# Kernel tuning notes

Measured on AMD Instinct MI355X. Metric: run time of the kernel, lower is better.

The kernel has to match this reference:

```python
import jax, jax.numpy as jnp
import numpy as np
from jax import lax

H_HEADS = 8      # attention heads
C_HID = 32       # per-head channels
NEG_SLOPE = 0.2  # PyG GATConv default leaky_relu slope


def _gat(x, src, dst, W, a_src, a_dst, b, num_nodes):
    # x: (N, Din); src/dst: (E',) with self-loops already appended
    h = (x @ W).reshape(num_nodes, H_HEADS, C_HID)          # (N, H, C)
    e = jax.nn.leaky_relu((h * a_src).sum(-1)[src] + (h * a_dst).sum(-1)[dst], NEG_SLOPE)  # (E', H)
    emax = jax.ops.segment_max(e, dst, num_segments=num_nodes)
    ex = jnp.exp(e - emax[dst])
    denom = jax.ops.segment_sum(ex, dst, num_segments=num_nodes)
    alpha = ex / (denom[dst] + 1e-16)                        # segment softmax over incoming edges
    out = jax.ops.segment_sum(h[src] * alpha[:, :, None], dst, num_segments=num_nodes)
    return out.reshape(num_nodes, H_HEADS * C_HID) + b


def _lstm_dir(seq, Wih, Whh, bih, bhh):
    # seq: (K, D); single-direction LSTM, returns final hidden state (Hs,)
    Hs = Whh.shape[1]
    def step(carry, x):
        h, c = carry
        g = x @ Wih.T + h @ Whh.T + bih + bhh                # (4*Hs,)
        i, f, gg, o = jnp.split(g, 4)
        c = jax.nn.sigmoid(f) * c + jax.nn.sigmoid(i) * jnp.tanh(gg)
        h = jax.nn.sigmoid(o) * jnp.tanh(c)
        return (h, c), None
    (h, _), _ = lax.scan(step, (jnp.zeros(Hs, seq.dtype), jnp.zeros(Hs, seq.dtype)), seq)
    return h


def setup_inputs():
    key = jax.random.key(0)
    ks = jax.random.split(key, 20)
    K, N, E = 8, 10000, 160000
    D1, D2, LH = 1, H_HEADS * C_HID, 256   # D2 = 256
    s = 0.1
    inp = {}
    inp['xs'] = jax.random.normal(ks[0], (K, N, D1), jnp.float32)
    inp['edge_index'] = jax.random.randint(ks[1], (K, 2, E), 0, N, jnp.int32)
    inp['W1'] = jax.random.normal(ks[2], (D1, D2), jnp.float32) * s
    inp['a_src1'] = jax.random.normal(ks[3], (H_HEADS, C_HID), jnp.float32) * s
    inp['a_dst1'] = jax.random.normal(ks[4], (H_HEADS, C_HID), jnp.float32) * s
    inp['b1'] = jnp.zeros((D2,), jnp.float32)
    inp['W2'] = jax.random.normal(ks[5], (D2, D2), jnp.float32) * s
    inp['a_src2'] = jax.random.normal(ks[6], (H_HEADS, C_HID), jnp.float32) * s
    inp['a_dst2'] = jax.random.normal(ks[7], (H_HEADS, C_HID), jnp.float32) * s
    inp['b2'] = jnp.zeros((D2,), jnp.float32)
    inp['Wih_f'] = jax.random.normal(ks[8], (4 * LH, D2), jnp.float32) * s
    inp['Whh_f'] = jax.random.normal(ks[9], (4 * LH, LH), jnp.float32) * s
    inp['bih_f'] = jnp.zeros((4 * LH,), jnp.float32)
    inp['bhh_f'] = jnp.zeros((4 * LH,), jnp.float32)
    inp['Wih_b'] = jax.random.normal(ks[10], (4 * LH, D2), jnp.float32) * s
    inp['Whh_b'] = jax.random.normal(ks[11], (4 * LH, LH), jnp.float32) * s
    inp['bih_b'] = jnp.zeros((4 * LH,), jnp.float32)
    inp['bhh_b'] = jnp.zeros((4 * LH,), jnp.float32)
    return inp


def reference(xs, edge_index, W1, a_src1, a_dst1, b1, W2, a_src2, a_dst2, b2,
              Wih_f, Whh_f, bih_f, bhh_f, Wih_b, Whh_b, bih_b, bhh_b):
    N = xs.shape[1]
    loops = jnp.arange(N, dtype=edge_index.dtype)  # self-loops (PyG default)
    def snap(carry, inp):
        x, ei = inp
        src = jnp.concatenate([ei[0], loops])
        dst = jnp.concatenate([ei[1], loops])
        h = jax.nn.relu(_gat(x, src, dst, W1, a_src1, a_dst1, b1, N))
        h = jax.nn.relu(_gat(h, src, dst, W2, a_src2, a_dst2, b2, N))
        return carry, h.mean(0)   # global mean pool -> (256,)
    _, embs = lax.scan(snap, 0, (xs, edge_index))   # (K, 256)
    h_fwd = _lstm_dir(embs, Wih_f, Whh_f, bih_f, bhh_f)
    h_bwd = _lstm_dir(embs[::-1], Wih_b, Whh_b, bih_b, bhh_b)
    return jnp.concatenate([h_fwd, h_bwd])[None, :]  # (1, 512)
```

## Files before the change

### kernel.cpp

```cpp
#include <hip/hip_runtime.h>
#include <math.h>

#define H_HEADS 8
#define C_HID 32
#define D2 256
#define NEG_SLOPE 0.2f
#define KSTEPS 8

__device__ __forceinline__ float lrelu(float x) { return x < 0.f ? NEG_SLOPE * x : x; }
__device__ __forceinline__ float sigmoidf(float x) { return 1.f / (1.f + expf(-x)); }


__global__ void zero_all_kernel(int* counts, int* fill, double* embp, int KN, int NEMBP,
                                const float* __restrict__ W1, const float* __restrict__ a_src1,
                                const float* __restrict__ a_dst1, float* Pvec, int D1) {
    int tid = blockIdx.x * blockDim.x + threadIdx.x;
    if (tid < KN) { counts[tid] = 0; fill[tid] = 0; }
    if (tid < NEMBP) embp[tid] = 0.0;
    if (blockIdx.x == 0 && threadIdx.x < 16 && D1 == 1) {
        int h = threadIdx.x & 7;
        const float* a = (threadIdx.x >= 8) ? a_dst1 : a_src1;
        float s = 0.f;
        for (int c = 0; c < 32; ++c) s += W1[h * 32 + c] * a[h * 32 + c];
        Pvec[threadIdx.x] = s;
    }
}


__global__ void count_all_kernel(const int* __restrict__ ei, int E, int N, int K,
                                 int* __restrict__ counts) {
    int bid = blockIdx.x;
    int k = bid % K;
    int jb = bid / K;
    int j = jb * blockDim.x + threadIdx.x;
    if (j >= E + N) return;
    int d = (j < E) ? ei[(size_t)k * 2 * E + E + j] : (j - E);
    atomicAdd(&counts[(size_t)k * N + d], 1);
}

__global__ __launch_bounds__(1024) void scan_all_kernel(const int* __restrict__ counts,
                                                        int* __restrict__ row_ptr, int N) {
    int k = blockIdx.x;
    const int* cnt = counts + (size_t)k * N;
    int* rp = row_ptr + (size_t)k * (N + 1);
    __shared__ int part[1024];
    int t = threadIdx.x;
    int ipt = (N + 1023) >> 10;
    int begin = t * ipt;
    int end = begin + ipt; if (end > N) end = N;
    if (begin > N) begin = N;
    int s = 0;
    for (int i = begin; i < end; ++i) s += cnt[i];
    part[t] = s;
    __syncthreads();
    for (int d = 1; d < 1024; d <<= 1) {
        int v = 0;
        if (t >= d) v = part[t - d];
        __syncthreads();
        if (t >= d) part[t] += v;
        __syncthreads();
    }
    int run = (t == 0) ? 0 : part[t - 1];
    for (int i = begin; i < end; ++i) { rp[i] = run; run += cnt[i]; }
    if (t == 1023) rp[N] = part[1023];
}

__global__ void scatter_all_kernel(const int* __restrict__ ei, int E, int N, int K,
                                   const int* __restrict__ row_ptr, int* __restrict__ fill,
                                   int* __restrict__ ein) {
    int bid = blockIdx.x;
    int k = bid % K;
    int jb = bid / K;
    int j = jb * blockDim.x + threadIdx.x;
    if (j >= E + N) return;
    int s, d;
    if (j < E) { s = ei[(size_t)k * 2 * E + j]; d = ei[(size_t)k * 2 * E + E + j]; }
    else { s = j - E; d = s; }
    int pos = row_ptr[(size_t)k * (N + 1) + d] + atomicAdd(&fill[(size_t)k * N + d], 1);
    ein[(size_t)k * (E + N) + pos] = s;
}


__global__ __launch_bounds__(256) void agg1_all_kernel(const float* __restrict__ xs,
                                                       const float* __restrict__ P,
                                                       const int* __restrict__ row_ptr,
                                                       const int* __restrict__ ein,
                                                       const float* __restrict__ W1,
                                                       const float* __restrict__ b1,
                                                       float* __restrict__ bufB,
                                                       int N, int E2, int k0, int BKcur) {
    int bid = blockIdx.x;
    int kb = bid % BKcur;
    int nb = bid / BKcur;
    int k = k0 + kb;
    const float* x = xs + (size_t)k * N;
    const int* rp = row_ptr + (size_t)k * (N + 1);
    const int* ek = ein + (size_t)k * E2;
    float* out = bufB + (size_t)kb * N * 256;

    int n = nb * 4 + (threadIdx.x >> 6);
    if (n >= N) return;
    int lane = threadIdx.x & 63;
    int e0 = rp[n], e1 = rp[n + 1];
    int h8 = lane & 7;
    float Ps = P[h8], Pd = P[8 + h8];
    float base = x[n] * Pd;

    float mx = -INFINITY;
    for (int i = e0 + (lane >> 3); i < e1; i += 8) {
        float xv = x[ek[i]];
        mx = fmaxf(mx, lrelu(xv * Ps + base));
    }
    mx = fmaxf(mx, __shfl_xor(mx, 8));
    mx = fmaxf(mx, __shfl_xor(mx, 16));
    mx = fmaxf(mx, __shfl_xor(mx, 32));

    float num = 0.f, den = 0.f;
    for (int i = e0 + (lane >> 3); i < e1; i += 8) {
        float xv = x[ek[i]];
        float w = expf(lrelu(xv * Ps + base) - mx);
        num += w * xv;
        den += w;
    }
    num += __shfl_xor(num, 8);  den += __shfl_xor(den, 8);
    num += __shfl_xor(num, 16); den += __shfl_xor(den, 16);
    num += __shfl_xor(num, 32); den += __shfl_xor(den, 32);
    float S = num / (den + 1e-16f);

    int hd = lane >> 3;
    float Sh = __shfl(S, hd);
    const float4 wv = *(const float4*)(W1 + lane * 4);
    const float4 bv = *(const float4*)(b1 + lane * 4);
    float4 o;
    o.x = fmaxf(Sh * wv.x + bv.x, 0.f);
    o.y = fmaxf(Sh * wv.y + bv.y, 0.f);
    o.z = fmaxf(Sh * wv.z + bv.z, 0.f);
    o.w = fmaxf(Sh * wv.w + bv.w, 0.f);
    *(float4*)(out + (size_t)n * 256 + lane * 4) = o;
}


__global__ void h1_kernel(const float* __restrict__ x, const float* __restrict__ W,
                          float* __restrict__ h, int N, int D1) {
    int tid = blockIdx.x * blockDim.x + threadIdx.x;
    if (tid >= N * 256) return;
    int n = tid >> 8, j = tid & 255;
    float acc = 0.f;
    for (int d = 0; d < D1; ++d) acc += x[n * D1 + d] * W[d * 256 + j];
    h[tid] = acc;
}

__global__ __launch_bounds__(256) void s_all_kernel(const float* __restrict__ bufA,
                                                    const float* __restrict__ a_src,
                                                    const float* __restrict__ a_dst,
                                                    float* __restrict__ s_src,
                                                    float* __restrict__ s_dst, int N) {
    int kb = blockIdx.y;
    int j = blockIdx.x * 256 + threadIdx.x;
    if (j >= N * 8) return;
    int n = j >> 3, hh = j & 7;
    const float* hp = bufA + (size_t)kb * N * 256 + (size_t)n * 256 + hh * 32;
    const float* as = a_src + hh * 32;
    const float* ad = a_dst + hh * 32;
    float ss = 0.f, sd = 0.f;
#pragma unroll
    for (int c = 0; c < 32; ++c) { float v = hp[c]; ss += v * as[c]; sd += v * ad[c]; }
    s_src[(size_t)kb * N * 8 + j] = ss;
    s_dst[(size_t)kb * N * 8 + j] = sd;
}

__global__ __launch_bounds__(256) void agg2_out_kernel(const float* __restrict__ h,
                                                       const float* __restrict__ s_src,
                                                       const float* __restrict__ s_dst,
                                                       const int* __restrict__ row_ptr,
                                                       const int* __restrict__ ein,
                                                       const float* __restrict__ bias,
                                                       float* __restrict__ out,
                                                       int N, int E2, int k0) {
    int k = k0;
    const int* rp = row_ptr + (size_t)k * (N + 1);
    const int* ek = ein + (size_t)k * E2;
    int n = blockIdx.x * 4 + (threadIdx.x >> 6);
    if (n >= N) return;
    int lane = threadIdx.x & 63;
    int e0 = rp[n], e1 = rp[n + 1];
    int h8 = lane & 7;
    float sd8 = s_dst[n * 8 + h8];

    float mx = -INFINITY;
    for (int i = e0 + (lane >> 3); i < e1; i += 8) {
        int s = ek[i];
        mx = fmaxf(mx, lrelu(s_src[s * 8 + h8] + sd8));
    }
    mx = fmaxf(mx, __shfl_xor(mx, 8));
    mx = fmaxf(mx, __shfl_xor(mx, 16));
    mx = fmaxf(mx, __shfl_xor(mx, 32));

    int hd = lane >> 3;
    float m = __shfl(mx, hd);
    float sdh = __shfl(sd8, hd);

    float den = 0.f;
    float4 acc = make_float4(0.f, 0.f, 0.f, 0.f);
    for (int i = e0; i < e1; ++i) {
        int s = ek[i];
        const float4 hv = *(const float4*)(h + (size_t)s * 256 + lane * 4);
        float w = expf(lrelu(s_src[s * 8 + hd] + sdh) - m);
        den += w;
        acc.x += w * hv.x; acc.y += w * hv.y; acc.z += w * hv.z; acc.w += w * hv.w;
    }
    float dE = den + 1e-16f;
    const float4 bv = *(const float4*)(bias + lane * 4);
    float4 o;
    o.x = fmaxf(acc.x / dE + bv.x, 0.f);
    o.y = fmaxf(acc.y / dE + bv.y, 0.f);
    o.z = fmaxf(acc.z / dE + bv.z, 0.f);
    o.w = fmaxf(acc.w / dE + bv.w, 0.f);
    *(float4*)(out + (size_t)n * 256 + lane * 4) = o;
}


__global__ __launch_bounds__(256) void agg2pool_kernel(const float* __restrict__ bufA,
                                                       const float* __restrict__ s_src,
                                                       const float* __restrict__ s_dst,
                                                       const int* __restrict__ row_ptr,
                                                       const int* __restrict__ ein,
                                                       const float* __restrict__ bias,
                                                       double* __restrict__ embp,
                                                       int N, int E2, int k0, int BKcur) {
    int bid = blockIdx.x;
    int kb = bid % BKcur;
    int nb = bid / BKcur;
    int k = k0 + kb;
    int w = threadIdx.x >> 6;
    int lane = threadIdx.x & 63;
    int n = nb * 4 + w;
    bool active = (n < N);
    const float* h = bufA + (size_t)kb * N * 256;
    const float* ssrc = s_src + (size_t)kb * N * 8;
    const float* sdst = s_dst + (size_t)kb * N * 8;
    const int* rp = row_ptr + (size_t)k * (N + 1);
    const int* ek = ein + (size_t)k * E2;

    float4 o = make_float4(0.f, 0.f, 0.f, 0.f);
    if (active) {
        int e0 = rp[n], e1 = rp[n + 1];
        int h8 = lane & 7;
        int es = lane >> 3;
        int hd = lane >> 3;
        float sd8 = sdst[n * 8 + h8];

        float mx = -INFINITY;
        for (int i = e0 + es; i < e1; i += 8) {
            int s = ek[i];
            mx = fmaxf(mx, lrelu(ssrc[s * 8 + h8] + sd8));
        }
        mx = fmaxf(mx, __shfl_xor(mx, 8));
        mx = fmaxf(mx, __shfl_xor(mx, 16));
        mx = fmaxf(mx, __shfl_xor(mx, 32));

        float den = 0.f;
        float4 acc = make_float4(0.f, 0.f, 0.f, 0.f);
        int hd4 = hd;

        for (int c0 = e0; c0 < e1; c0 += 8) {
            int eI = c0 + es;
            bool valid = (eI < e1);
            int sA = ek[valid ? eI : e0];
            float wv = expf(lrelu(ssrc[sA * 8 + h8] + sd8) - mx);
            if (!valid) wv = 0.f;

            int jmax = e1 - c0; if (jmax > 8) jmax = 8;
#pragma unroll 8
            for (int j = 0; j < 8; ++j) {
                if (j >= jmax) break;
                int srcLane = (j << 3) + hd4;
                float wj = __shfl(wv, srcLane);
                int sj = __shfl(sA, srcLane);
                const float4 hv = *(const float4*)(h + (size_t)sj * 256 + lane * 4);
                den += wj;
                acc.x += wj * hv.x;
                acc.y += wj * hv.y;
                acc.z += wj * hv.z;
                acc.w += wj * hv.w;
            }
        }
        float dE = den + 1e-16f;
        const float4 bv = *(const float4*)(bias + lane * 4);
        o.x = fmaxf(acc.x / dE + bv.x, 0.f);
        o.y = fmaxf(acc.y / dE + bv.y, 0.f);
        o.z = fmaxf(acc.z / dE + bv.z, 0.f);
        o.w = fmaxf(acc.w / dE + bv.w, 0.f);
    }

    __shared__ double pe[4][256];
    pe[w][lane * 4 + 0] = (double)o.x;
    pe[w][lane * 4 + 1] = (double)o.y;
    pe[w][lane * 4 + 2] = (double)o.z;
    pe[w][lane * 4 + 3] = (double)o.w;
    __syncthreads();
    int tid = threadIdx.x;
    double s = pe[0][tid] + pe[1][tid] + pe[2][tid] + pe[3][tid];
    atomicAdd(&embp[((size_t)k * 32 + (nb & 31)) * 256 + tid], s);
}


__global__ __launch_bounds__(256) void gemm_kernel(const float* __restrict__ A,
                                                   const float* __restrict__ B,
                                                   float* __restrict__ C, int M) {
    __shared__ float Ast[8][132];
    __shared__ float Bs[8][128];
    int tid = threadIdx.x;
    int bm = blockIdx.x, bn = blockIdx.y;
    int ty = tid >> 4, tx = tid & 15;
    int r0 = ty * 8, c0 = tx * 8;
    float acc[8][8] = {};
    int arow = tid >> 1, acol = (tid & 1) * 4;
    int brow = tid >> 5, bcol = (tid & 31) * 4;
    const float* Bbase = B + bn * 128;

    for (int kt = 0; kt < 256; kt += 8) {
        int gr = bm * 128 + arow;
        float4 av = (gr < M) ? *(const float4*)(A + (size_t)gr * 256 + kt + acol)
                             : make_float4(0.f, 0.f, 0.f, 0.f);
        Ast[acol + 0][arow] = av.x;
        Ast[acol + 1][arow] = av.y;
        Ast[acol + 2][arow] = av.z;
        Ast[acol + 3][arow] = av.w;
        *(float4*)&Bs[brow][bcol] = *(const float4*)(Bbase + (size_t)(kt + brow) * 256 + bcol);
        __syncthreads();
#pragma unroll
        for (int kk = 0; kk < 8; ++kk) {
            float4 a0 = *(const float4*)&Ast[kk][r0];
            float4 a1 = *(const float4*)&Ast[kk][r0 + 4];
            float4 b0 = *(const float4*)&Bs[kk][c0];
            float4 b1 = *(const float4*)&Bs[kk][c0 + 4];
            float ar[8] = {a0.x, a0.y, a0.z, a0.w, a1.x, a1.y, a1.z, a1.w};
            float br[8] = {b0.x, b0.y, b0.z, b0.w, b1.x, b1.y, b1.z, b1.w};
#pragma unroll
            for (int i2 = 0; i2 < 8; ++i2)
#pragma unroll
                for (int j2 = 0; j2 < 8; ++j2) acc[i2][j2] += ar[i2] * br[j2];
        }
        __syncthreads();
    }
#pragma unroll
    for (int i2 = 0; i2 < 8; ++i2) {
        int gm = bm * 128 + r0 + i2;
        if (gm < M) {
            *(float4*)(C + (size_t)gm * 256 + bn * 128 + c0) =
                make_float4(acc[i2][0], acc[i2][1], acc[i2][2], acc[i2][3]);
            *(float4*)(C + (size_t)gm * 256 + bn * 128 + c0 + 4) =
                make_float4(acc[i2][4], acc[i2][5], acc[i2][6], acc[i2][7]);
        }
    }
}


__global__ void merge_kernel(const double* __restrict__ embp, float* __restrict__ emb,
                             int* __restrict__ flags) {
    int k = blockIdx.x, c = threadIdx.x;
    double s = 0.0;
#pragma unroll
    for (int p = 0; p < 32; ++p) s += embp[((size_t)k * 32 + p) * 256 + c];
    emb[k * 256 + c] = (float)s;
    if (blockIdx.x == 0 && threadIdx.x < 2 * (KSTEPS + 1)) flags[threadIdx.x] = 0;
}


__global__ __launch_bounds__(256) void lstm_rec_kernel(
    const float* __restrict__ emb, float invN,
    const float* __restrict__ Wih_f, const float* __restrict__ Whh_f,
    const float* __restrict__ bih_f, const float* __restrict__ bhh_f,
    const float* __restrict__ Wih_b, const float* __restrict__ Whh_b,
    const float* __restrict__ bih_b, const float* __restrict__ bhh_b,
    float* __restrict__ hbuf,
    int* __restrict__ flags,
    float* __restrict__ out) {
    int dir = blockIdx.x >> 4;
    int seg = blockIdx.x & 15;
    const float* Wih = dir ? Wih_b : Wih_f;
    const float* Whh = dir ? Whh_b : Whh_f;
    const float* bih = dir ? bih_b : bih_f;
    const float* bhh = dir ? bhh_b : bhh_f;

    __shared__ float wh[64 * 256];
    __shared__ float wi[64 * 256];
    __shared__ float xs_s[KSTEPS * 256];
    __shared__ float gx[KSTEPS][64];
    __shared__ float garr[64];
    __shared__ float hprev_s[256];
    int tid = threadIdx.x;

    for (int v = tid; v < 64 * 64; v += 256) {
        int lrow = v >> 6;
        int c4 = (v & 63) * 4;
        int grow = ((lrow >> 4) << 8) + seg * 16 + (lrow & 15);
        *(float4*)&wh[lrow * 256 + c4] = *(const float4*)(Whh + (size_t)grow * 256 + c4);
        *(float4*)&wi[lrow * 256 + c4] = *(const float4*)(Wih + (size_t)grow * 256 + c4);
    }
    for (int idx = tid; idx < KSTEPS * 256; idx += 256) xs_s[idx] = emb[idx] * invN;
    __syncthreads();

    for (int d = tid; d < KSTEPS * 64; d += 256) {
        int st = d >> 6, lr = d & 63;
        const float* wr = &wi[lr << 8];
        const float* xr = &xs_s[st << 8];
        int r = (tid & 63) << 2;
        float acc = 0.f;
#pragma unroll 8
        for (int kk = 0; kk < 256; kk += 4) {
            int k2 = (kk + r) & 255;
            acc += wr[k2] * xr[k2] + wr[k2 + 1] * xr[k2 + 1] +
                   wr[k2 + 2] * xr[k2 + 2] + wr[k2 + 3] * xr[k2 + 3];
        }
        int grow = ((lr >> 4) << 8) + seg * 16 + (lr & 15);
        gx[st][lr] = acc + bih[grow] + bhh[grow];
    }

    int* flag = flags + dir * (KSTEPS + 1);
    float* hb = hbuf + dir * (KSTEPS + 1) * 256;

    if (tid < 16)
        __hip_atomic_store(&hb[seg * 16 + tid], 0.f, __ATOMIC_RELAXED, __HIP_MEMORY_SCOPE_AGENT);
    __syncthreads();
    if (tid == 0)
        __hip_atomic_fetch_add(&flag[0], 1, __ATOMIC_RELEASE, __HIP_MEMORY_SCOPE_AGENT);

    float c_reg = 0.f;

    for (int step = 0; step < KSTEPS; ++step) {
        if (tid == 0) {
            while (__hip_atomic_load(&flag[step], __ATOMIC_RELAXED, __HIP_MEMORY_SCOPE_AGENT) < 16) {
                __builtin_amdgcn_s_sleep(1);
            }
            (void)__hip_atomic_load(&flag[step], __ATOMIC_ACQUIRE, __HIP_MEMORY_SCOPE_AGENT);
        }
        __syncthreads();
        hprev_s[tid] = __hip_atomic_load(&hb[step * 256 + tid], __ATOMIC_RELAXED,
                                         __HIP_MEMORY_SCOPE_AGENT);
        __syncthreads();

        int d = tid >> 2, p = tid & 3;
        const float* wr = &wh[(d << 8) + (p << 6)];
        const float* hr = &hprev_s[p << 6];
        int rot = tid & 63;
        float acc = 0.f;
#pragma unroll 8
        for (int k = 0; k < 64; ++k) {
            int k2 = (k + rot) & 63;
            acc += wr[k2] * hr[k2];
        }
        acc += __shfl_xor(acc, 1);
        acc += __shfl_xor(acc, 2);
        if (p == 0) garr[d] = acc;
        __syncthreads();

        if (tid < 16) {
            float ig = sigmoidf(garr[tid] + gx[step][tid]);
            float fg = sigmoidf(garr[16 + tid] + gx[step][16 + tid]);
            float gg = tanhf(garr[32 + tid] + gx[step][32 + tid]);
            float og = sigmoidf(garr[48 + tid] + gx[step][48 + tid]);
            float cn = fg * c_reg + ig * gg;
            c_reg = cn;
            float hn = og * tanhf(cn);
            __hip_atomic_store(&hb[(step + 1) * 256 + seg * 16 + tid], hn, __ATOMIC_RELAXED,
                               __HIP_MEMORY_SCOPE_AGENT);
        }
        __syncthreads();
        if (tid == 0)
            __hip_atomic_fetch_add(&flag[step + 1], 1, __ATOMIC_RELEASE, __HIP_MEMORY_SCOPE_AGENT);
    }

    if (tid < 16)
        out[dir * 256 + seg * 16 + tid] =
            __hip_atomic_load(&hb[KSTEPS * 256 + seg * 16 + tid], __ATOMIC_RELAXED,
                              __HIP_MEMORY_SCOPE_AGENT);
}


extern "C" void kernel_launch(void* const* d_in, const int* in_sizes, int n_in,
                              void* d_out, int out_size, void* d_ws, size_t ws_size,
                              hipStream_t stream) {
    const float* xs = (const float*)d_in[0];
    const int* edge_index = (const int*)d_in[1];
    const float* W1 = (const float*)d_in[2];
    const float* a_src1 = (const float*)d_in[3];
    const float* a_dst1 = (const float*)d_in[4];
    const float* b1 = (const float*)d_in[5];
    const float* W2 = (const float*)d_in[6];
    const float* a_src2 = (const float*)d_in[7];
    const float* a_dst2 = (const float*)d_in[8];
    const float* b2 = (const float*)d_in[9];
    const float* Wih_f = (const float*)d_in[10];
    const float* Whh_f = (const float*)d_in[11];
    const float* bih_f = (const float*)d_in[12];
    const float* bhh_f = (const float*)d_in[13];
    const float* Wih_b = (const float*)d_in[14];
    const float* Whh_b = (const float*)d_in[15];
    const float* bih_b = (const float*)d_in[16];
    const float* bhh_b = (const float*)d_in[17];

    const int K = KSTEPS;
    int D1 = in_sizes[2] / D2;
    int N = in_sizes[0] / (K * D1);
    int E = in_sizes[1] / (2 * K);
    int E2 = E + N;

    auto al = [](size_t x) { return (x + 255) & ~(size_t)255; };
    size_t fixed_sz = al((size_t)K * N * 4)
                    + al((size_t)K * (N + 1) * 4)
                    + al((size_t)K * N * 4)
                    + al((size_t)K * E2 * 4)
                    + al((size_t)K * 32 * 256 * 8)
                    + al((size_t)K * 256 * 4)
                    + al((size_t)2 * (K + 1) * 256 * 4)
                    + al((size_t)2 * (K + 1) * 4)
                    + al(16 * 4);
    int BK = 8;
    while (BK > 1) {
        size_t need = fixed_sz + 2 * al((size_t)BK * N * 8 * 4) + 2 * al((size_t)BK * N * 256 * 4);
        if (need <= ws_size) break;
        BK >>= 1;
    }

    char* w = (char*)d_ws;
    auto alloc = [&](size_t bytes) { char* p = w; w += (bytes + 255) & ~(size_t)255; return p; };
    int* counts = (int*)alloc((size_t)K * N * 4);
    int* row_ptr = (int*)alloc((size_t)K * (N + 1) * 4);
    int* fill = (int*)alloc((size_t)K * N * 4);
    int* ein = (int*)alloc((size_t)K * E2 * 4);
    double* embp = (double*)alloc((size_t)K * 32 * 256 * 8);
    float* emb = (float*)alloc((size_t)K * 256 * 4);
    float* hbuf = (float*)alloc((size_t)2 * (K + 1) * 256 * 4);
    int* flags = (int*)alloc((size_t)2 * (K + 1) * 4);
    float* Pvec = (float*)alloc(16 * 4);
    float* s_src = (float*)alloc((size_t)BK * N * 8 * 4);
    float* s_dst = (float*)alloc((size_t)BK * N * 8 * 4);
    float* bufA = (float*)alloc((size_t)BK * N * 256 * 4);
    float* bufB = (float*)alloc((size_t)BK * N * 256 * 4);

    int KN = K * N;
    int NEMBP = K * 32 * 256;
    int zblk = ((KN > NEMBP ? KN : NEMBP) + 255) / 256;
    zero_all_kernel<<<zblk, 256, 0, stream>>>(counts, fill, embp, KN, NEMBP,
                                              W1, a_src1, a_dst1, Pvec, D1);
    int eblk = (E2 + 255) / 256;
    count_all_kernel<<<eblk * K, 256, 0, stream>>>(edge_index, E, N, K, counts);
    scan_all_kernel<<<K, 1024, 0, stream>>>(counts, row_ptr, N);
    scatter_all_kernel<<<eblk * K, 256, 0, stream>>>(edge_index, E, N, K, row_ptr, fill, ein);

    int nblk4 = (N + 3) / 4;
    int sblk = (N * 8 + 255) / 256;
    for (int k0 = 0; k0 < K; k0 += BK) {
        int BKcur = (K - k0 < BK) ? (K - k0) : BK;
        if (D1 == 1) {
            agg1_all_kernel<<<nblk4 * BKcur, 256, 0, stream>>>(
                xs, Pvec, row_ptr, ein, W1, b1, bufB, N, E2, k0, BKcur);
            int M = BKcur * N;
            gemm_kernel<<<dim3((M + 127) / 128, 2), 256, 0, stream>>>(bufB, W2, bufA, M);
            s_all_kernel<<<dim3(sblk, BKcur), 256, 0, stream>>>(bufA, a_src2, a_dst2,
                                                                s_src, s_dst, N);
            agg2pool_kernel<<<nblk4 * BKcur, 256, 0, stream>>>(
                bufA, s_src, s_dst, row_ptr, ein, b2, embp, N, E2, k0, BKcur);
        } else {
            for (int kk = 0; kk < BKcur; ++kk) {
                int k = k0 + kk;
                const float* xk = xs + (size_t)k * N * D1;
                h1_kernel<<<(N * 256 + 255) / 256, 256, 0, stream>>>(xk, W1, bufA, N, D1);
                s_all_kernel<<<dim3(sblk, 1), 256, 0, stream>>>(bufA, a_src1, a_dst1,
                                                                s_src, s_dst, N);
                agg2_out_kernel<<<nblk4, 256, 0, stream>>>(bufA, s_src, s_dst, row_ptr, ein,
                                                           b1, bufB, N, E2, k);
                gemm_kernel<<<dim3((N + 127) / 128, 2), 256, 0, stream>>>(bufB, W2, bufA, N);
                s_all_kernel<<<dim3(sblk, 1), 256, 0, stream>>>(bufA, a_src2, a_dst2,
                                                                s_src, s_dst, N);
                agg2pool_kernel<<<nblk4, 256, 0, stream>>>(
                    bufA, s_src, s_dst, row_ptr, ein, b2, embp, N, E2, k, 1);
            }
        }
    }

    merge_kernel<<<K, 256, 0, stream>>>(embp, emb, flags);
    lstm_rec_kernel<<<32, 256, 0, stream>>>(emb, 1.f / (float)N,
                                            Wih_f, Whh_f, bih_f, bhh_f,
                                            Wih_b, Whh_b, bih_b, bhh_b,
                                            hbuf, flags, (float*)d_out);
}
```

Before: 613.4 us.

## Fuse layer-1 rank-1 expansion into layer-2 GEMM prologue via compact per-head scalars

The first GAT layer now writes only 8 per-head aggregated scalars per node instead of the full 256-wide relu(S*W1+b1) activation. The second-layer GEMM rebuilds the A tile on the fly from those scalars, W1 and b1 held in shared memory. The aim is to avoid writing and re-reading a K*N*256 float intermediate in global memory. The GEMM also switches to a 16-deep k-tile with a per-wave quadrant layout, which adds ALU work in the tile-load stage and uses more shared memory.

```diff
diff --git a/kernel.cpp b/kernel.cpp
--- a/kernel.cpp
+++ b/kernel.cpp
@@ -81,14 +81,12 @@
 }
 
 
-__global__ __launch_bounds__(256) void agg1_all_kernel(const float* __restrict__ xs,
-                                                       const float* __restrict__ P,
-                                                       const int* __restrict__ row_ptr,
-                                                       const int* __restrict__ ein,
-                                                       const float* __restrict__ W1,
-                                                       const float* __restrict__ b1,
-                                                       float* __restrict__ bufB,
-                                                       int N, int E2, int k0, int BKcur) {
+__global__ __launch_bounds__(256) void agg1s_all_kernel(const float* __restrict__ xs,
+                                                        const float* __restrict__ P,
+                                                        const int* __restrict__ row_ptr,
+                                                        const int* __restrict__ ein,
+                                                        float* __restrict__ Sbuf,
+                                                        int N, int E2, int k0, int BKcur) {
     int bid = blockIdx.x;
     int kb = bid % BKcur;
     int nb = bid / BKcur;
@@ -96,7 +94,6 @@
     const float* x = xs + (size_t)k * N;
     const int* rp = row_ptr + (size_t)k * (N + 1);
     const int* ek = ein + (size_t)k * E2;
-    float* out = bufB + (size_t)kb * N * 256;
 
     int n = nb * 4 + (threadIdx.x >> 6);
     if (n >= N) return;
@@ -127,16 +124,7 @@
     num += __shfl_xor(num, 32); den += __shfl_xor(den, 32);
     float S = num / (den + 1e-16f);
 
-    int hd = lane >> 3;
-    float Sh = __shfl(S, hd);
-    const float4 wv = *(const float4*)(W1 + lane * 4);
-    const float4 bv = *(const float4*)(b1 + lane * 4);
-    float4 o;
-    o.x = fmaxf(Sh * wv.x + bv.x, 0.f);
-    o.y = fmaxf(Sh * wv.y + bv.y, 0.f);
-    o.z = fmaxf(Sh * wv.z + bv.z, 0.f);
-    o.w = fmaxf(Sh * wv.w + bv.w, 0.f);
-    *(float4*)(out + (size_t)n * 256 + lane * 4) = o;
+    if (lane < 8) Sbuf[((size_t)kb * N + n) * 8 + lane] = S;
 }
 
 
@@ -305,6 +293,85 @@
 }
 
 
+__global__ __launch_bounds__(256) void gemm_fused_kernel(const float* __restrict__ S,
+                                                         const float* __restrict__ W1,
+                                                         const float* __restrict__ bias1,
+                                                         const float* __restrict__ B,
+                                                         float* __restrict__ C, int M) {
+    __shared__ float Ast[16][132];
+    __shared__ float Bs[16][132];
+    __shared__ float w1s[256], b1s[256];
+    __shared__ float Ss[128 * 8];
+    int tid = threadIdx.x;
+    int bm = blockIdx.x, bn = blockIdx.y;
+
+    w1s[tid] = W1[tid];
+    b1s[tid] = bias1[tid];
+    {
+        int base = bm * 128 * 8 + tid * 4;
+        float4 sv = make_float4(0.f, 0.f, 0.f, 0.f);
+        if (bm * 128 + (tid * 4) / 8 < M) {
+            sv = *(const float4*)(S + base);
+        }
+        *(float4*)&Ss[tid * 4] = sv;
+    }
+
+    int arow = tid >> 1;
+    int kgrp = (tid & 1) * 8;
+    bool rowvalid = (bm * 128 + arow < M);
+
+    int brow = tid >> 4;
+    int bcol = (tid & 15) * 8;
+    const float* Bbase = B + bn * 128;
+
+    int w = tid >> 6, lane = tid & 63;
+    int qr = (w >> 1) * 64, qc = (w & 1) * 64;
+    int ty = lane >> 3, tx = lane & 7;
+    int r0 = qr + ty * 8, c0 = qc + tx * 8;
+    float acc[8][8] = {};
+
+    __syncthreads();
+
+    for (int kt = 0; kt < 256; kt += 16) {
+        float sh = Ss[arow * 8 + (kt >> 5)];
+#pragma unroll
+        for (int j = 0; j < 8; ++j) {
+            int kk = kgrp + j;
+            float a = fmaxf(fmaf(sh, w1s[kt + kk], b1s[kt + kk]), 0.f);
+            Ast[kk][arow] = rowvalid ? a : 0.f;
+        }
+        const float* bg = Bbase + (size_t)(kt + brow) * 256 + bcol;
+        *(float4*)&Bs[brow][bcol] = *(const float4*)bg;
+        *(float4*)&Bs[brow][bcol + 4] = *(const float4*)(bg + 4);
+        __syncthreads();
+#pragma unroll
+        for (int kk = 0; kk < 16; ++kk) {
+            float4 a0 = *(const float4*)&Ast[kk][r0];
+            float4 a1 = *(const float4*)&Ast[kk][r0 + 4];
+            float4 b0 = *(const float4*)&Bs[kk][c0];
+            float4 b1v = *(const float4*)&Bs[kk][c0 + 4];
+            float ar[8] = {a0.x, a0.y, a0.z, a0.w, a1.x, a1.y, a1.z, a1.w};
+            float br[8] = {b0.x, b0.y, b0.z, b0.w, b1v.x, b1v.y, b1v.z, b1v.w};
+#pragma unroll
+            for (int i2 = 0; i2 < 8; ++i2)
+#pragma unroll
+                for (int j2 = 0; j2 < 8; ++j2) acc[i2][j2] += ar[i2] * br[j2];
+        }
+        __syncthreads();
+    }
+#pragma unroll
+    for (int i2 = 0; i2 < 8; ++i2) {
+        int gm = bm * 128 + r0 + i2;
+        if (gm < M) {
+            *(float4*)(C + (size_t)gm * 256 + bn * 128 + c0) =
+                make_float4(acc[i2][0], acc[i2][1], acc[i2][2], acc[i2][3]);
+            *(float4*)(C + (size_t)gm * 256 + bn * 128 + c0 + 4) =
+                make_float4(acc[i2][4], acc[i2][5], acc[i2][6], acc[i2][7]);
+        }
+    }
+}
+
+
 __global__ __launch_bounds__(256) void gemm_kernel(const float* __restrict__ A,
                                                    const float* __restrict__ B,
                                                    float* __restrict__ C, int M) {
@@ -374,9 +441,7 @@
     const float* __restrict__ bih_f, const float* __restrict__ bhh_f,
     const float* __restrict__ Wih_b, const float* __restrict__ Whh_b,
     const float* __restrict__ bih_b, const float* __restrict__ bhh_b,
-    float* __restrict__ hbuf,
-    int* __restrict__ flags,
-    float* __restrict__ out) {
+    float* __restrict__ hbuf, int* __restrict__ flags, float* __restrict__ out) {
     int dir = blockIdx.x >> 4;
     int seg = blockIdx.x & 15;
     const float* Wih = dir ? Wih_b : Wih_f;
@@ -519,7 +584,7 @@
                     + al(16 * 4);
     int BK = 8;
     while (BK > 1) {
-        size_t need = fixed_sz + 2 * al((size_t)BK * N * 8 * 4) + 2 * al((size_t)BK * N * 256 * 4);
+        size_t need = fixed_sz + 3 * al((size_t)BK * N * 8 * 4) + 2 * al((size_t)BK * N * 256 * 4);
         if (need <= ws_size) break;
         BK >>= 1;
     }
@@ -535,6 +600,7 @@
     float* hbuf = (float*)alloc((size_t)2 * (K + 1) * 256 * 4);
     int* flags = (int*)alloc((size_t)2 * (K + 1) * 4);
     float* Pvec = (float*)alloc(16 * 4);
+    float* Sbuf = (float*)alloc((size_t)BK * N * 8 * 4);
     float* s_src = (float*)alloc((size_t)BK * N * 8 * 4);
     float* s_dst = (float*)alloc((size_t)BK * N * 8 * 4);
     float* bufA = (float*)alloc((size_t)BK * N * 256 * 4);
@@ -555,10 +621,11 @@
     for (int k0 = 0; k0 < K; k0 += BK) {
         int BKcur = (K - k0 < BK) ? (K - k0) : BK;
         if (D1 == 1) {
-            agg1_all_kernel<<<nblk4 * BKcur, 256, 0, stream>>>(
-                xs, Pvec, row_ptr, ein, W1, b1, bufB, N, E2, k0, BKcur);
+            agg1s_all_kernel<<<nblk4 * BKcur, 256, 0, stream>>>(
+                xs, Pvec, row_ptr, ein, Sbuf, N, E2, k0, BKcur);
             int M = BKcur * N;
-            gemm_kernel<<<dim3((M + 127) / 128, 2), 256, 0, stream>>>(bufB, W2, bufA, M);
+            gemm_fused_kernel<<<dim3((M + 127) / 128, 2), 256, 0, stream>>>(
+                Sbuf, W1, b1, W2, bufA, M);
             s_all_kernel<<<dim3(sblk, BKcur), 256, 0, stream>>>(bufA, a_src2, a_dst2,
                                                                 s_src, s_dst, N);
             agg2pool_kernel<<<nblk4 * BKcur, 256, 0, stream>>>(
```

Result: faster. 582.8 us (-5.0%).
